# Performance work log

Measured on AMD Instinct MI355X. Metric: run time of the kernel, lower is better.

The kernel has to match this reference:

```python
import jax, jax.numpy as jnp
import numpy as np

N_NODES = 50000
N_EDGES = 600000
F_IN = 128
HID = 128
LN_EPS = 1e-5


def setup_inputs() -> dict:
    key = jax.random.key(0)
    ks = jax.random.split(key, 8)
    x = jax.random.normal(ks[0], (N_NODES, F_IN), dtype=jnp.float32)
    edge_index = jax.random.randint(ks[1], (2, N_EDGES), 0, N_NODES, dtype=jnp.int64)
    s1 = 1.0 / np.sqrt(F_IN)
    s2 = 1.0 / np.sqrt(HID)
    return {
        "x": x,
        "edge_index": edge_index,
        "W1": jax.random.normal(ks[2], (F_IN, HID), dtype=jnp.float32) * s1,
        "b1": jnp.zeros((HID,), dtype=jnp.float32),
        "g1": jnp.ones((HID,), dtype=jnp.float32),
        "be1": jnp.zeros((HID,), dtype=jnp.float32),
        "W2": jax.random.normal(ks[3], (HID, HID), dtype=jnp.float32) * s2,
        "b2": jnp.zeros((HID,), dtype=jnp.float32),
        "g2": jnp.ones((HID,), dtype=jnp.float32),
        "be2": jnp.zeros((HID,), dtype=jnp.float32),
    }


def _layer_norm(h, g, b):
    mu = jnp.mean(h, axis=-1, keepdims=True)
    var = jnp.mean(jnp.square(h - mu), axis=-1, keepdims=True)
    return (h - mu) * jax.lax.rsqrt(var + LN_EPS) * g + b


def reference(x, edge_index, W1, b1, g1, be1, W2, b2, g2, be2):
    n = x.shape[0]
    src, dst = edge_index[0], edge_index[1]
    # GCN symmetric normalization with self-loops: deg = in-degree(A) + 1
    deg = jax.ops.segment_sum(jnp.ones_like(src, dtype=x.dtype), dst, num_segments=n) + 1.0
    dinv = jax.lax.rsqrt(deg)                       # D^{-1/2}, [N]
    enorm = (dinv[src] * dinv[dst])[:, None]        # per-edge norm, [E,1]
    self_norm = (dinv * dinv)[:, None]              # self-loop norm,  [N,1]

    def gcn(h, W, b):
        h = h @ W                                   # [N,HID]
        agg = jax.ops.segment_sum(h[src] * enorm, dst, num_segments=n)
        return agg + h * self_norm + b

    h = jax.nn.relu(_layer_norm(gcn(x, W1, b1), g1, be1))
    h = jax.nn.relu(_layer_norm(gcn(h, W2, b2), g2, be2))
    return h  # dropout is identity in eval; LSTM evolution only runs in training
```

## Files before the change

### kernel.cpp

```cpp
#include <hip/hip_runtime.h>

#define N_NODES 50000
#define N_EDGES 600000
#define HID 128
#define LN_EPS 1e-5f
#define MAXDEG 64
#define NB_GEMM1 782
#define NB_PLACE 2344

typedef __attribute__((ext_vector_type(8))) short short8;
typedef __attribute__((ext_vector_type(4))) float f32x4;

__device__ inline float b2f(unsigned short u) {
    union { unsigned int i; float f; } v;
    v.i = ((unsigned int)u) << 16;
    return v.f;
}
__device__ inline unsigned short f2b(float f) {
    union { float f; unsigned int u; } v; v.f = f;
    unsigned int r = (v.u + 0x7FFFu + ((v.u >> 16) & 1u)) >> 16;
    return (unsigned short)r;
}

__global__ __launch_bounds__(256) void k_fused1(const float* __restrict__ x,
                                                const float* __restrict__ W1,
                                                const float* __restrict__ W2,
                                                const int* __restrict__ ei,
                                                int* __restrict__ cursor,
                                                int* __restrict__ esrc,
                                                unsigned short* __restrict__ WT2,
                                                unsigned short* __restrict__ hb) {
    const int tid = threadIdx.x;

    if (blockIdx.x >= NB_GEMM1) {
        const int bi = blockIdx.x - NB_GEMM1;
        const int e = bi * 256 + tid;
        if (e < N_EDGES) {
            const int d = ei[N_EDGES + e];
            const int pos = atomicAdd(&cursor[d], 1);
            if (pos < MAXDEG) esrc[d * MAXDEG + pos] = ei[e];
        }
        if (bi < 64) {
            const int i = bi * 256 + tid;
            const int k = i >> 7, n = i & 127;
            WT2[n * 128 + k] = f2b(W2[i]);
        }
        return;
    }

    __shared__ unsigned short wt[16384];
    {
        const float4* W4 = (const float4*)W1;
#pragma unroll
        for (int it = 0; it < 16; ++it) {
            const int i4 = tid + 256 * it;
            const float4 v = W4[i4];
            const int k  = (i4 * 4) >> 7;
            const int n0 = (i4 * 4) & 127;
            wt[(n0 + 0) * 128 + (k ^ (((n0 + 0) & 7) << 3))] = f2b(v.x);
            wt[(n0 + 1) * 128 + (k ^ (((n0 + 1) & 7) << 3))] = f2b(v.y);
            wt[(n0 + 2) * 128 + (k ^ (((n0 + 2) & 7) << 3))] = f2b(v.z);
            wt[(n0 + 3) * 128 + (k ^ (((n0 + 3) & 7) << 3))] = f2b(v.w);
        }
    }
    __syncthreads();

    const int lane = tid & 63;
    const int ln   = lane & 15;
    const int quad = lane >> 4;
    const int m0   = blockIdx.x * 64 + (tid >> 6) * 16;

    f32x4 acc[8];
#pragma unroll
    for (int t = 0; t < 8; ++t) acc[t] = (f32x4){0.f, 0.f, 0.f, 0.f};

    int arow = m0 + ln;
    if (arow >= N_NODES) arow = N_NODES - 1;
    const float* aptr = x + (size_t)arow * HID + quad * 8;

#pragma unroll
    for (int ks = 0; ks < 4; ++ks) {
        const float4 v0 = *(const float4*)(aptr + ks * 32);
        const float4 v1 = *(const float4*)(aptr + ks * 32 + 4);
        short8 a;
        a[0] = (short)f2b(v0.x); a[1] = (short)f2b(v0.y);
        a[2] = (short)f2b(v0.z); a[3] = (short)f2b(v0.w);
        a[4] = (short)f2b(v1.x); a[5] = (short)f2b(v1.y);
        a[6] = (short)f2b(v1.z); a[7] = (short)f2b(v1.w);
#pragma unroll
        for (int t = 0; t < 8; ++t) {
            const int n = t * 16 + ln;
            const short8 b = *(const short8*)&wt[n * 128 + ((quad * 8 + ks * 32) ^ ((n & 7) << 3))];
            acc[t] = __builtin_amdgcn_mfma_f32_16x16x32_bf16(a, b, acc[t], 0, 0, 0);
        }
    }

#pragma unroll
    for (int t = 0; t < 8; ++t) {
#pragma unroll
        for (int r = 0; r < 4; ++r) {
            const int row = m0 + quad * 4 + r;
            if (row < N_NODES) hb[(size_t)row * HID + t * 16 + ln] = f2b(acc[t][r]);
        }
    }
}

template <bool FUSE>
__global__ __launch_bounds__(256) void k_agg(const int* __restrict__ cursor,
                                             const int* __restrict__ esrc,
                                             const unsigned short* __restrict__ h,
                                             const float* __restrict__ bia,
                                             const float* __restrict__ g,
                                             const float* __restrict__ be,
                                             const unsigned short* __restrict__ WT2,
                                             unsigned short* __restrict__ hb2,
                                             float* __restrict__ outf) {
    __shared__ unsigned short tile[2048];
    const int tid  = threadIdx.x;
    const int wv   = tid >> 6;
    const int lane = tid & 63;
    const int grp  = lane >> 4;
    const int fl   = lane & 15;
    const int r    = wv * 4 + grp;
    const int row  = blockIdx.x * 16 + r;

    const int cntA = cursor[row];
    const int cnt  = cntA < MAXDEG ? cntA : MAXDEG;
    const int e0   = row * MAXDEG;
    const int e1   = e0 + cnt;

    float acc[8];
#pragma unroll
    for (int j = 0; j < 8; ++j) acc[j] = 0.f;

    int e = e0;
    for (; e + 3 < e1; e += 4) {
        const int4 s4 = *(const int4*)(esrc + e);
        const float w0 = rsqrtf((float)cursor[s4.x] + 1.0f);
        const float w1 = rsqrtf((float)cursor[s4.y] + 1.0f);
        const float w2 = rsqrtf((float)cursor[s4.z] + 1.0f);
        const float w3 = rsqrtf((float)cursor[s4.w] + 1.0f);
        const short8 v0 = *(const short8*)(h + (size_t)s4.x * HID + 8 * fl);
        const short8 v1 = *(const short8*)(h + (size_t)s4.y * HID + 8 * fl);
        const short8 v2 = *(const short8*)(h + (size_t)s4.z * HID + 8 * fl);
        const short8 v3 = *(const short8*)(h + (size_t)s4.w * HID + 8 * fl);
#pragma unroll
        for (int j = 0; j < 8; ++j) {
            acc[j] = fmaf(w0, b2f((unsigned short)v0[j]), acc[j]);
            acc[j] = fmaf(w1, b2f((unsigned short)v1[j]), acc[j]);
            acc[j] = fmaf(w2, b2f((unsigned short)v2[j]), acc[j]);
            acc[j] = fmaf(w3, b2f((unsigned short)v3[j]), acc[j]);
        }
    }
    for (; e < e1; ++e) {
        const int sA = esrc[e];
        const float wA = rsqrtf((float)cursor[sA] + 1.0f);
        const short8 vA = *(const short8*)(h + (size_t)sA * HID + 8 * fl);
#pragma unroll
        for (int j = 0; j < 8; ++j)
            acc[j] = fmaf(wA, b2f((unsigned short)vA[j]), acc[j]);
    }

    const float dd = rsqrtf((float)cntA + 1.0f);
    const float sn = dd * dd;
    const short8 hv = *(const short8*)(h + (size_t)row * HID + 8 * fl);
    const float4 b0 = *(const float4*)(bia + 8 * fl);
    const float4 b1 = *(const float4*)(bia + 8 * fl + 4);
    const float bb[8] = {b0.x, b0.y, b0.z, b0.w, b1.x, b1.y, b1.z, b1.w};

    float v[8], s = 0.f, ss = 0.f;
#pragma unroll
    for (int j = 0; j < 8; ++j) {
        v[j] = dd * acc[j] + b2f((unsigned short)hv[j]) * sn + bb[j];
        s += v[j];
        ss = fmaf(v[j], v[j], ss);
    }

#pragma unroll
    for (int off = 1; off <= 8; off <<= 1) {
        s  += __shfl_xor(s, off);
        ss += __shfl_xor(ss, off);
    }
    const float mu  = s * (1.0f / 128.0f);
    const float var = ss * (1.0f / 128.0f) - mu * mu;
    const float rs  = rsqrtf(var + LN_EPS);

    const float4 g0  = *(const float4*)(g + 8 * fl);
    const float4 g1  = *(const float4*)(g + 8 * fl + 4);
    const float4 e0v = *(const float4*)(be + 8 * fl);
    const float4 e1v = *(const float4*)(be + 8 * fl + 4);
    const float gg[8] = {g0.x, g0.y, g0.z, g0.w, g1.x, g1.y, g1.z, g1.w};
    const float ee[8] = {e0v.x, e0v.y, e0v.z, e0v.w, e1v.x, e1v.y, e1v.z, e1v.w};
    float o[8];
#pragma unroll
    for (int j = 0; j < 8; ++j)
        o[j] = fmaxf((v[j] - mu) * rs * gg[j] + ee[j], 0.0f);

    if constexpr (!FUSE) {
        float4 w0 = {o[0], o[1], o[2], o[3]};
        float4 w1 = {o[4], o[5], o[6], o[7]};
        *(float4*)(outf + (size_t)row * HID + 8 * fl) = w0;
        *(float4*)(outf + (size_t)row * HID + 8 * fl + 4) = w1;
    } else {
        short8 w;
#pragma unroll
        for (int j = 0; j < 8; ++j) w[j] = (short)f2b(o[j]);
        *(short8*)&tile[r * 128 + ((8 * fl) ^ ((r & 7) << 3))] = w;
        __syncthreads();

        f32x4 c0 = (f32x4){0.f, 0.f, 0.f, 0.f};
        f32x4 c1 = (f32x4){0.f, 0.f, 0.f, 0.f};
        const int n0 = (wv * 2) * 16 + fl;
#pragma unroll
        for (int ks = 0; ks < 4; ++ks) {
            const short8 a = *(const short8*)&tile[fl * 128 + ((grp * 8 + ks * 32) ^ ((fl & 7) << 3))];
            const short8 bf0 = *(const short8*)(WT2 + (size_t)n0 * HID + grp * 8 + ks * 32);
            c0 = __builtin_amdgcn_mfma_f32_16x16x32_bf16(a, bf0, c0, 0, 0, 0);
            const short8 bf1 = *(const short8*)(WT2 + (size_t)(n0 + 16) * HID + grp * 8 + ks * 32);
            c1 = __builtin_amdgcn_mfma_f32_16x16x32_bf16(a, bf1, c1, 0, 0, 0);
        }
#pragma unroll
        for (int rr = 0; rr < 4; ++rr) {
            const int orow = blockIdx.x * 16 + grp * 4 + rr;
            hb2[(size_t)orow * HID + n0]      = f2b(c0[rr]);
            hb2[(size_t)orow * HID + n0 + 16] = f2b(c1[rr]);
        }
    }
}

extern "C" void kernel_launch(void* const* d_in, const int* in_sizes, int n_in,
                              void* d_out, int out_size, void* d_ws, size_t ws_size,
                              hipStream_t stream) {
    (void)in_sizes; (void)n_in; (void)out_size; (void)ws_size;

    const float* x   = (const float*)d_in[0];
    const int*   ei  = (const int*)d_in[1];
    const float* W1  = (const float*)d_in[2];
    const float* b1  = (const float*)d_in[3];
    const float* g1  = (const float*)d_in[4];
    const float* be1 = (const float*)d_in[5];
    const float* W2  = (const float*)d_in[6];
    const float* b2  = (const float*)d_in[7];
    const float* g2  = (const float*)d_in[8];
    const float* be2 = (const float*)d_in[9];
    float* out = (float*)d_out;

    int* cursor = (int*)d_ws;
    int* esrc   = (int*)d_ws + 50016;
    unsigned short* WT2 = (unsigned short*)((int*)d_ws + 3250016);
    unsigned short* hb  = (unsigned short*)((int*)d_ws + 3258208);
    unsigned short* hb2 = (unsigned short*)((int*)d_ws + 6458208);

    hipMemsetAsync(cursor, 0, N_NODES * sizeof(int), stream);
    k_fused1<<<NB_GEMM1 + NB_PLACE, 256, 0, stream>>>(x, W1, W2, ei, cursor, esrc, WT2, hb);

    k_agg<true><<<N_NODES / 16, 256, 0, stream>>>(cursor, esrc, hb, b1, g1, be1, WT2, hb2, nullptr);
    k_agg<false><<<N_NODES / 16, 256, 0, stream>>>(cursor, esrc, hb2, b2, g2, be2, nullptr, nullptr, out);
}
```

Measured before the change: 190.4 us.

## Split each row's edge gather across two half-blocks with LDS reduction

Aggregation blocks double from 256 to 512 threads. The two halves each gather a different half of a row's neighbor list and combine their partial sums through shared memory before LayerNorm. The fused layer-2 GEMM is then spread over 8 waves, each computing one 16-column tile. The goal is more memory-level parallelism and shorter per-thread latency chains in the gather. The cost is extra syncthreads, an LDS round trip, and idle threads in the LN stage.

Result: no change. 188.7 us (-0.9%).

```diff
diff --git a/kernel.cpp b/kernel.cpp
--- a/kernel.cpp
+++ b/kernel.cpp
@@ -106,35 +106,39 @@
 }
 
 template <bool FUSE>
-__global__ __launch_bounds__(256) void k_agg(const int* __restrict__ cursor,
-                                             const int* __restrict__ esrc,
-                                             const unsigned short* __restrict__ h,
-                                             const float* __restrict__ bia,
-                                             const float* __restrict__ g,
-                                             const float* __restrict__ be,
-                                             const unsigned short* __restrict__ WT2,
-                                             unsigned short* __restrict__ hb2,
-                                             float* __restrict__ outf) {
-    __shared__ unsigned short tile[2048];
+__device__ __forceinline__ void agg_body(const int* __restrict__ cursor,
+                                         const int* __restrict__ esrc,
+                                         const unsigned short* __restrict__ h,
+                                         const float* __restrict__ bia,
+                                         const float* __restrict__ g,
+                                         const float* __restrict__ be,
+                                         const unsigned short* __restrict__ WT2,
+                                         unsigned short* __restrict__ hb2,
+                                         float* __restrict__ outf) {
+    __shared__ float pbuf[2048];
     const int tid  = threadIdx.x;
     const int wv   = tid >> 6;
     const int lane = tid & 63;
     const int grp  = lane >> 4;
     const int fl   = lane & 15;
-    const int r    = wv * 4 + grp;
+    const int half = wv >> 2;
+    const int r    = (wv & 3) * 4 + grp;
     const int row  = blockIdx.x * 16 + r;
 
-    const int cntA = cursor[row];
-    const int cnt  = cntA < MAXDEG ? cntA : MAXDEG;
-    const int e0   = row * MAXDEG;
-    const int e1   = e0 + cnt;
+    const int cntA  = cursor[row];
+    const int cnt   = cntA < MAXDEG ? cntA : MAXDEG;
+    const int ebase = row * MAXDEG;
+    const int c0    = ((cnt + 7) >> 3) << 2;
+    const int h0n   = c0 < cnt ? c0 : cnt;
+    const int eb    = half ? ebase + h0n : ebase;
+    const int ee    = half ? ebase + cnt : ebase + h0n;
 
     float acc[8];
 #pragma unroll
     for (int j = 0; j < 8; ++j) acc[j] = 0.f;
 
-    int e = e0;
-    for (; e + 3 < e1; e += 4) {
+    int e = eb;
+    for (; e + 3 < ee; e += 4) {
         const int4 s4 = *(const int4*)(esrc + e);
         const float w0 = rsqrtf((float)cursor[s4.x] + 1.0f);
         const float w1 = rsqrtf((float)cursor[s4.y] + 1.0f);
@@ -152,7 +156,7 @@
             acc[j] = fmaf(w3, b2f((unsigned short)v3[j]), acc[j]);
         }
     }
-    for (; e < e1; ++e) {
+    for (; e < ee; ++e) {
         const int sA = esrc[e];
         const float wA = rsqrtf((float)cursor[sA] + 1.0f);
         const short8 vA = *(const short8*)(h + (size_t)sA * HID + 8 * fl);
@@ -161,71 +165,104 @@
             acc[j] = fmaf(wA, b2f((unsigned short)vA[j]), acc[j]);
     }
 
-    const float dd = rsqrtf((float)cntA + 1.0f);
-    const float sn = dd * dd;
-    const short8 hv = *(const short8*)(h + (size_t)row * HID + 8 * fl);
-    const float4 b0 = *(const float4*)(bia + 8 * fl);
-    const float4 b1 = *(const float4*)(bia + 8 * fl + 4);
-    const float bb[8] = {b0.x, b0.y, b0.z, b0.w, b1.x, b1.y, b1.z, b1.w};
-
-    float v[8], s = 0.f, ss = 0.f;
-#pragma unroll
-    for (int j = 0; j < 8; ++j) {
-        v[j] = dd * acc[j] + b2f((unsigned short)hv[j]) * sn + bb[j];
-        s += v[j];
-        ss = fmaf(v[j], v[j], ss);
-    }
-
-#pragma unroll
-    for (int off = 1; off <= 8; off <<= 1) {
-        s  += __shfl_xor(s, off);
-        ss += __shfl_xor(ss, off);
-    }
-    const float mu  = s * (1.0f / 128.0f);
-    const float var = ss * (1.0f / 128.0f) - mu * mu;
-    const float rs  = rsqrtf(var + LN_EPS);
-
-    const float4 g0  = *(const float4*)(g + 8 * fl);
-    const float4 g1  = *(const float4*)(g + 8 * fl + 4);
-    const float4 e0v = *(const float4*)(be + 8 * fl);
-    const float4 e1v = *(const float4*)(be + 8 * fl + 4);
-    const float gg[8] = {g0.x, g0.y, g0.z, g0.w, g1.x, g1.y, g1.z, g1.w};
-    const float ee[8] = {e0v.x, e0v.y, e0v.z, e0v.w, e1v.x, e1v.y, e1v.z, e1v.w};
+    if (half == 1) {
+#pragma unroll
+        for (int j = 0; j < 8; ++j) pbuf[r * 128 + 8 * fl + j] = acc[j];
+    }
+    __syncthreads();
+
     float o[8];
-#pragma unroll
-    for (int j = 0; j < 8; ++j)
-        o[j] = fmaxf((v[j] - mu) * rs * gg[j] + ee[j], 0.0f);
+    if (half == 0) {
+#pragma unroll
+        for (int j = 0; j < 8; ++j) acc[j] += pbuf[r * 128 + 8 * fl + j];
+
+        const float dd = rsqrtf((float)cntA + 1.0f);
+        const float sn = dd * dd;
+        const short8 hv = *(const short8*)(h + (size_t)row * HID + 8 * fl);
+        const float4 b0 = *(const float4*)(bia + 8 * fl);
+        const float4 b1 = *(const float4*)(bia + 8 * fl + 4);
+        const float bb[8] = {b0.x, b0.y, b0.z, b0.w, b1.x, b1.y, b1.z, b1.w};
+
+        float v[8], s = 0.f, ss = 0.f;
+#pragma unroll
+        for (int j = 0; j < 8; ++j) {
+            v[j] = dd * acc[j] + b2f((unsigned short)hv[j]) * sn + bb[j];
+            s += v[j];
+            ss = fmaf(v[j], v[j], ss);
+        }
+#pragma unroll
+        for (int off = 1; off <= 8; off <<= 1) {
+            s  += __shfl_xor(s, off);
+            ss += __shfl_xor(ss, off);
+        }
+        const float mu  = s * (1.0f / 128.0f);
+        const float var = ss * (1.0f / 128.0f) - mu * mu;
+        const float rs  = rsqrtf(var + LN_EPS);
+
+        const float4 g0  = *(const float4*)(g + 8 * fl);
+        const float4 g1  = *(const float4*)(g + 8 * fl + 4);
+        const float4 e0v = *(const float4*)(be + 8 * fl);
+        const float4 e1v = *(const float4*)(be + 8 * fl + 4);
+        const float gg[8] = {g0.x, g0.y, g0.z, g0.w, g1.x, g1.y, g1.z, g1.w};
+        const float ee2[8] = {e0v.x, e0v.y, e0v.z, e0v.w, e1v.x, e1v.y, e1v.z, e1v.w};
+#pragma unroll
+        for (int j = 0; j < 8; ++j)
+            o[j] = fmaxf((v[j] - mu) * rs * gg[j] + ee2[j], 0.0f);
+    }
 
     if constexpr (!FUSE) {
-        float4 w0 = {o[0], o[1], o[2], o[3]};
-        float4 w1 = {o[4], o[5], o[6], o[7]};
-        *(float4*)(outf + (size_t)row * HID + 8 * fl) = w0;
-        *(float4*)(outf + (size_t)row * HID + 8 * fl + 4) = w1;
+        if (half == 0) {
+            float4 w0 = {o[0], o[1], o[2], o[3]};
+            float4 w1 = {o[4], o[5], o[6], o[7]};
+            *(float4*)(outf + (size_t)row * HID + 8 * fl) = w0;
+            *(float4*)(outf + (size_t)row * HID + 8 * fl + 4) = w1;
+        }
     } else {
-        short8 w;
-#pragma unroll
-        for (int j = 0; j < 8; ++j) w[j] = (short)f2b(o[j]);
-        *(short8*)&tile[r * 128 + ((8 * fl) ^ ((r & 7) << 3))] = w;
         __syncthreads();
-
-        f32x4 c0 = (f32x4){0.f, 0.f, 0.f, 0.f};
-        f32x4 c1 = (f32x4){0.f, 0.f, 0.f, 0.f};
-        const int n0 = (wv * 2) * 16 + fl;
+        unsigned short* tile = (unsigned short*)pbuf;
+        if (half == 0) {
+            short8 w;
+#pragma unroll
+            for (int j = 0; j < 8; ++j) w[j] = (short)f2b(o[j]);
+            *(short8*)&tile[r * 128 + ((8 * fl) ^ ((r & 7) << 3))] = w;
+        }
+        __syncthreads();
+
+        f32x4 c = (f32x4){0.f, 0.f, 0.f, 0.f};
+        const int n0 = wv * 16 + fl;
 #pragma unroll
         for (int ks = 0; ks < 4; ++ks) {
-            const short8 a = *(const short8*)&tile[fl * 128 + ((grp * 8 + ks * 32) ^ ((fl & 7) << 3))];
-            const short8 bf0 = *(const short8*)(WT2 + (size_t)n0 * HID + grp * 8 + ks * 32);
-            c0 = __builtin_amdgcn_mfma_f32_16x16x32_bf16(a, bf0, c0, 0, 0, 0);
-            const short8 bf1 = *(const short8*)(WT2 + (size_t)(n0 + 16) * HID + grp * 8 + ks * 32);
-            c1 = __builtin_amdgcn_mfma_f32_16x16x32_bf16(a, bf1, c1, 0, 0, 0);
+            const short8 a  = *(const short8*)&tile[fl * 128 + ((grp * 8 + ks * 32) ^ ((fl & 7) << 3))];
+            const short8 bf = *(const short8*)(WT2 + (size_t)n0 * HID + grp * 8 + ks * 32);
+            c = __builtin_amdgcn_mfma_f32_16x16x32_bf16(a, bf, c, 0, 0, 0);
         }
 #pragma unroll
         for (int rr = 0; rr < 4; ++rr) {
             const int orow = blockIdx.x * 16 + grp * 4 + rr;
-            hb2[(size_t)orow * HID + n0]      = f2b(c0[rr]);
-            hb2[(size_t)orow * HID + n0 + 16] = f2b(c1[rr]);
-        }
-    }
+            hb2[(size_t)orow * HID + n0] = f2b(c[rr]);
+        }
+    }
+}
+
+__global__ __launch_bounds__(512, 4) void k_agg_fuse(const int* __restrict__ cursor,
+                                                     const int* __restrict__ esrc,
+                                                     const unsigned short* __restrict__ h,
+                                                     const float* __restrict__ bia,
+                                                     const float* __restrict__ g,
+                                                     const float* __restrict__ be,
+                                                     const unsigned short* __restrict__ WT2,
+                                                     unsigned short* __restrict__ hb2) {
+    agg_body<true>(cursor, esrc, h, bia, g, be, WT2, hb2, nullptr);
+}
+
+__global__ __launch_bounds__(512, 4) void k_agg_out(const int* __restrict__ cursor,
+                                                    const int* __restrict__ esrc,
+                                                    const unsigned short* __restrict__ h,
+                                                    const float* __restrict__ bia,
+                                                    const float* __restrict__ g,
+                                                    const float* __restrict__ be,
+                                                    float* __restrict__ outf) {
+    agg_body<false>(cursor, esrc, h, bia, g, be, nullptr, nullptr, outf);
 }
 
 extern "C" void kernel_launch(void* const* d_in, const int* in_sizes, int n_in,
@@ -254,6 +291,6 @@
     hipMemsetAsync(cursor, 0, N_NODES * sizeof(int), stream);
     k_fused1<<<NB_GEMM1 + NB_PLACE, 256, 0, stream>>>(x, W1, W2, ei, cursor, esrc, WT2, hb);
 
-    k_agg<true><<<N_NODES / 16, 256, 0, stream>>>(cursor, esrc, hb, b1, g1, be1, WT2, hb2, nullptr);
-    k_agg<false><<<N_NODES / 16, 256, 0, stream>>>(cursor, esrc, hb2, b2, g2, be2, nullptr, nullptr, out);
-}
+    k_agg_fuse<<<N_NODES / 16, 512, 0, stream>>>(cursor, esrc, hb, b1, g1, be1, WT2, hb2);
+    k_agg_out<<<N_NODES / 16, 512, 0, stream>>>(cursor, esrc, hb2, b2, g2, be2, out);
+}
```
